# Kernel tuning notes

Measured on AMD Instinct MI355X. Metric: run time of the kernel, lower is better.

The kernel has to match this reference:

```python
import jax, jax.numpy as jnp
import numpy as np

MIN_SIGMA = 1e-3  # min_sigma from __init__
EPS = 1e-16


def rbf_kernel(A, B, sigma):
    """A: (bs, n, d), B: (m, d) -> K: (bs, n, m) with K = exp(-||a-b||^2 / (2 sigma^2))."""
    s = jnp.maximum(sigma, MIN_SIGMA)
    a2 = jnp.sum(A * A, axis=-1, keepdims=True)              # (bs, n, 1)
    b2 = jnp.sum(B * B, axis=-1)                             # (m,)
    d2 = a2 + b2[None, None, :] - 2.0 * jnp.einsum('bnd,md->bnm', A, B)
    d2 = jnp.maximum(d2, 0.0)
    return jnp.exp(-d2 / (2.0 * s * s))


def setup_inputs() -> dict:
    key = jax.random.key(0)
    k1, k2, k3 = jax.random.split(key, 3)
    BS, N, DX, DY, M = 256, 128, 32, 10, 2048  # batch, items(bag), dim_x, dim_y, n_comp
    inputs = jax.random.normal(k1, (BS, N, DX), dtype=jnp.float32)
    c_x = jax.random.normal(k2, (M, DX), dtype=jnp.float32)
    c_y = jax.random.uniform(k3, (M, DY), dtype=jnp.float32)
    comp_w = jnp.full((M,), 1.0 / M, dtype=jnp.float32)
    # sigma chosen ~ sqrt(dim_x) so RBF values don't underflow for Gaussian inputs
    sigma = jnp.float32(8.0)
    return {"inputs": inputs, "sigma": sigma, "c_x": c_x, "c_y": c_y, "comp_w": comp_w}


def reference(inputs, sigma, c_x, c_y, comp_w):
    bs, n, _ = inputs.shape
    # comp2dm: uniform bag weights w, components = inputs
    w = jnp.full((bs, n), 1.0 / n, dtype=inputs.dtype)       # (bs, n)
    # KQMUnit: kernel measurement
    K = rbf_kernel(inputs, c_x, sigma)                        # (bs, n, n_comp)
    out_w = jnp.einsum('bn,bnm->bm', w, comp_w[None, None, :] * (K * K))  # (bs, n_comp)
    out_w_sum = jnp.sum(out_w, axis=-1, keepdims=True)
    y_w = out_w / jnp.where(out_w_sum == 0, EPS, out_w_sum)   # normalized mixture weights
    # dm2comp + row-normalize components (batch-independent c_y)
    y_v = c_y / jnp.linalg.norm(c_y, axis=-1, keepdims=True)  # (n_comp, dim_y)
    # probs = einsum('...j,...ji->...i', y_w, y_v**2)
    probs = jnp.einsum('bm,md->bd', y_w, y_v * y_v)           # (bs, dim_y)
    return probs
```

## Files before the change

kernel.cpp:

```cpp
#include <hip/hip_runtime.h>
#include <hip/hip_bf16.h>

#define BS     256
#define N_BAG  128
#define DXD    32
#define DYD    10
#define M_COMP 2048
#define NTILES 8
#define WAVES  16
#define MT_PW  8

typedef __attribute__((ext_vector_type(8))) short short8v;
typedef __attribute__((ext_vector_type(4))) float f32x4;

static __device__ __forceinline__ unsigned int pkbf(float a, float b) {
    unsigned short ha = __bfloat16_as_ushort(__float2bfloat16(a));
    unsigned short hb = __bfloat16_as_ushort(__float2bfloat16(b));
    return (unsigned int)ha | ((unsigned int)hb << 16);
}
static __device__ __forceinline__ float fast_exp2(float x) {
#if __has_builtin(__builtin_amdgcn_exp2f)
    return __builtin_amdgcn_exp2f(x);
#else
    return __expf(x * 0.6931471805599453f);
#endif
}

__global__ __launch_bounds__(1024, 4) void fused_kernel(
    const float* __restrict__ X,
    const float* __restrict__ sig_p,
    const float* __restrict__ c_x,
    const float* __restrict__ c_y,
    const float* __restrict__ comp_w,
    float* __restrict__ out)
{
    __shared__ short8v XhiF[NTILES][64];
    __shared__ float   a2part[N_BAG][4];
    __shared__ float   a2buf[N_BAG];
    __shared__ float   red[WAVES][DYD + 2];
    __shared__ float   sm[DYD + 1];

    const int tid = threadIdx.x;
    const int b   = blockIdx.x;

    if (tid < 512) {
        const int n = tid >> 2, g4 = tid & 3;
        const float4* Xr = (const float4*)(X + ((size_t)(b * N_BAG + n) * DXD + 8 * g4));
        float4 v0 = Xr[0], v1 = Xr[1];
        float s = 0.f;
        s = fmaf(v0.x, v0.x, s); s = fmaf(v0.y, v0.y, s);
        s = fmaf(v0.z, v0.z, s); s = fmaf(v0.w, v0.w, s);
        s = fmaf(v1.x, v1.x, s); s = fmaf(v1.y, v1.y, s);
        s = fmaf(v1.z, v1.z, s); s = fmaf(v1.w, v1.w, s);
        union { unsigned int u[4]; short8v s8; } cv;
        cv.u[0] = pkbf(v0.x, v0.y); cv.u[1] = pkbf(v0.z, v0.w);
        cv.u[2] = pkbf(v1.x, v1.y); cv.u[3] = pkbf(v1.z, v1.w);
        XhiF[n >> 4][g4 * 16 + (n & 15)] = cv.s8;
        a2part[n][g4] = s;
    }
    __syncthreads();
    if (tid < N_BAG)
        a2buf[tid] = -0.5f * (a2part[tid][0] + a2part[tid][1] +
                              a2part[tid][2] + a2part[tid][3]);
    __syncthreads();

    const int lane = tid & 63, wv = tid >> 6;
    const int r = lane & 15, gq = lane >> 4;
    const int rowg = gq * 4;
    short8v Ah[NTILES];
    f32x4   a2f[NTILES];
#pragma unroll
    for (int t = 0; t < NTILES; ++t) {
        Ah[t]  = XhiF[t][lane];
        a2f[t] = *(const f32x4*)&a2buf[t * 16 + rowg];
    }

    const float sgm = fmaxf(sig_p[0], 1e-3f);
    const float cp  = 2.0f * 1.4426950408889634f / (sgm * sgm);

    float acc11[DYD + 1];
#pragma unroll
    for (int v = 0; v <= DYD; ++v) acc11[v] = 0.f;

    const int    m_base = wv * (MT_PW * 16) + r;
    const float* cxp    = c_x + (size_t)m_base * DXD + 8 * gq;

    float4 p0 = *(const float4*)(cxp);
    float4 p1 = *(const float4*)(cxp + 4);

#pragma unroll
    for (int i = 0; i < MT_PW; ++i) {
        const int m = m_base + 16 * i;
        float4 q0, q1;
        if (i + 1 < MT_PW) {
            q0 = *(const float4*)(cxp + (i + 1) * 16 * DXD);
            q1 = *(const float4*)(cxp + (i + 1) * 16 * DXD + 4);
        }
        const float cw = comp_w[m] * (1.0f / N_BAG);
        float cy[DYD];
        if (lane < 16) {
#pragma unroll
            for (int d = 0; d < DYD; ++d) cy[d] = c_y[(size_t)m * DYD + d];
        }
        union { unsigned int u[4]; short8v s8; } bc;
        bc.u[0] = pkbf(p0.x, p0.y); bc.u[1] = pkbf(p0.z, p0.w);
        bc.u[2] = pkbf(p1.x, p1.y); bc.u[3] = pkbf(p1.z, p1.w);
        float s = 0.f;
        s = fmaf(p0.x, p0.x, s); s = fmaf(p0.y, p0.y, s);
        s = fmaf(p0.z, p0.z, s); s = fmaf(p0.w, p0.w, s);
        s = fmaf(p1.x, p1.x, s); s = fmaf(p1.y, p1.y, s);
        s = fmaf(p1.z, p1.z, s); s = fmaf(p1.w, p1.w, s);
        s += __shfl_xor(s, 16, 64);
        s += __shfl_xor(s, 32, 64);
        const float cb = -0.5f * cp * s;

        float csum = 0.f;
#pragma unroll
        for (int t = 0; t < NTILES; ++t) {
            f32x4 acc = __builtin_amdgcn_mfma_f32_16x16x32_bf16(Ah[t], bc.s8, a2f[t], 0, 0, 0);
#pragma unroll
            for (int rr = 0; rr < 4; ++rr) {
                float e = fminf(fmaf(cp, acc[rr], cb), 0.f);
                csum += fast_exp2(e);
            }
        }
        csum += __shfl_xor(csum, 16, 64);
        csum += __shfl_xor(csum, 32, 64);

        if (lane < 16) {
            float ny = 0.f;
#pragma unroll
            for (int d = 0; d < DYD; ++d) ny = fmaf(cy[d], cy[d], ny);
            const float owm = csum * cw;
            const float yw  = owm * __builtin_amdgcn_rcpf(ny);
            acc11[0] += owm;
#pragma unroll
            for (int d = 0; d < DYD; ++d)
                acc11[1 + d] = fmaf(cy[d] * cy[d], yw, acc11[1 + d]);
        }
        p0 = q0; p1 = q1;
    }

#pragma unroll
    for (int v = 0; v <= DYD; ++v) {
        float x = acc11[v];
#pragma unroll
        for (int off = 32; off > 0; off >>= 1) x += __shfl_down(x, off, 64);
        if (lane == 0) red[wv][v] = x;
    }
    __syncthreads();
    if (tid <= DYD) {
        float ssum = 0.f;
#pragma unroll
        for (int w = 0; w < WAVES; ++w) ssum += red[w][tid];
        sm[tid] = ssum;
    }
    __syncthreads();
    if (tid < DYD) {
        float d = sm[0];
        d = (d == 0.f) ? 1e-16f : d;
        out[(size_t)b * DYD + tid] = sm[1 + tid] / d;
    }
}

extern "C" void kernel_launch(void* const* d_in, const int* in_sizes, int n_in,
                              void* d_out, int out_size, void* d_ws, size_t ws_size,
                              hipStream_t stream) {
    const float* X      = (const float*)d_in[0];
    const float* sigma  = (const float*)d_in[1];
    const float* c_x    = (const float*)d_in[2];
    const float* c_y    = (const float*)d_in[3];
    const float* comp_w = (const float*)d_in[4];
    float*       out    = (float*)d_out;

    fused_kernel<<<BS, 1024, 0, stream>>>(X, sigma, c_x, c_y, comp_w, out);
}
```

Before: 25.68 us.

## Split component dimension across blocks with two-kernel partial-sum reduction

Launches 8 blocks of 256 threads per batch row, each covering a 256-component chunk instead of one 1024-thread block per row, then combines per-chunk partial sums in a second small kernel. The scale and bias are folded into the bf16 A operand and the MFMA accumulator seed, which removes the per-element fma and clamp before exp2. The c_y reduction is moved to one component per thread with coalesced loads. This aims at better occupancy and load balance, at the cost of recomputing X prep per chunk, an extra launch, and dropping the clamp of the squared distance at zero.

```diff
diff --git a/kernel.cpp b/kernel.cpp
--- a/kernel.cpp
+++ b/kernel.cpp
@@ -6,9 +6,7 @@
 #define DXD    32
 #define DYD    10
 #define M_COMP 2048
-#define NTILES 8
-#define WAVES  16
-#define MT_PW  8
+#define CHUNKS 8
 
 typedef __attribute__((ext_vector_type(8))) short short8v;
 typedef __attribute__((ext_vector_type(4))) float f32x4;
@@ -26,25 +24,33 @@
 #endif
 }
 
-__global__ __launch_bounds__(1024, 4) void fused_kernel(
+__global__ __launch_bounds__(256, 8) void main_kernel(
     const float* __restrict__ X,
     const float* __restrict__ sig_p,
     const float* __restrict__ c_x,
     const float* __restrict__ c_y,
     const float* __restrict__ comp_w,
-    float* __restrict__ out)
+    float* __restrict__ part)
 {
-    __shared__ short8v XhiF[NTILES][64];
+    __shared__ short8v Af[8][64];
     __shared__ float   a2part[N_BAG][4];
-    __shared__ float   a2buf[N_BAG];
-    __shared__ float   red[WAVES][DYD + 2];
-    __shared__ float   sm[DYD + 1];
+    __shared__ float   a2c[N_BAG];
+    __shared__ float   ow_s[2][256];
+    __shared__ float   red[4][12];
 
-    const int tid = threadIdx.x;
-    const int b   = blockIdx.x;
+    const int tid   = threadIdx.x;
+    const int bid   = blockIdx.x;
+    const int b     = bid >> 3;
+    const int chunk = bid & 7;
 
-    if (tid < 512) {
-        const int n = tid >> 2, g4 = tid & 3;
+    const float sgm = fmaxf(sig_p[0], 1e-3f);
+    const float c2  = -1.4426950408889634f / (sgm * sgm);
+    const float sA  = -2.0f * c2;
+
+#pragma unroll
+    for (int k = 0; k < 2; ++k) {
+        const int u = tid + 256 * k;
+        const int n = u >> 2, g4 = u & 3;
         const float4* Xr = (const float4*)(X + ((size_t)(b * N_BAG + n) * DXD + 8 * g4));
         float4 v0 = Xr[0], v1 = Xr[1];
         float s = 0.f;
@@ -52,59 +58,39 @@
         s = fmaf(v0.z, v0.z, s); s = fmaf(v0.w, v0.w, s);
         s = fmaf(v1.x, v1.x, s); s = fmaf(v1.y, v1.y, s);
         s = fmaf(v1.z, v1.z, s); s = fmaf(v1.w, v1.w, s);
-        union { unsigned int u[4]; short8v s8; } cv;
-        cv.u[0] = pkbf(v0.x, v0.y); cv.u[1] = pkbf(v0.z, v0.w);
-        cv.u[2] = pkbf(v1.x, v1.y); cv.u[3] = pkbf(v1.z, v1.w);
-        XhiF[n >> 4][g4 * 16 + (n & 15)] = cv.s8;
+        union { unsigned int u4[4]; short8v s8; } cv;
+        cv.u4[0] = pkbf(sA * v0.x, sA * v0.y); cv.u4[1] = pkbf(sA * v0.z, sA * v0.w);
+        cv.u4[2] = pkbf(sA * v1.x, sA * v1.y); cv.u4[3] = pkbf(sA * v1.z, sA * v1.w);
+        Af[n >> 4][g4 * 16 + (n & 15)] = cv.s8;
         a2part[n][g4] = s;
     }
     __syncthreads();
     if (tid < N_BAG)
-        a2buf[tid] = -0.5f * (a2part[tid][0] + a2part[tid][1] +
-                              a2part[tid][2] + a2part[tid][3]);
+        a2c[tid] = c2 * (a2part[tid][0] + a2part[tid][1] +
+                         a2part[tid][2] + a2part[tid][3]);
     __syncthreads();
 
     const int lane = tid & 63, wv = tid >> 6;
-    const int r = lane & 15, gq = lane >> 4;
-    const int rowg = gq * 4;
-    short8v Ah[NTILES];
-    f32x4   a2f[NTILES];
+    const int half = wv & 1, wp = wv >> 1;
+    const int r = lane & 15, gq = lane >> 4, rowg = gq * 4;
+
+    short8v Xf[4];
+    f32x4   s4[4];
 #pragma unroll
-    for (int t = 0; t < NTILES; ++t) {
-        Ah[t]  = XhiF[t][lane];
-        a2f[t] = *(const f32x4*)&a2buf[t * 16 + rowg];
+    for (int j = 0; j < 4; ++j) {
+        Xf[j] = Af[half * 4 + j][lane];
+        s4[j] = *(const f32x4*)&a2c[(half * 4 + j) * 16 + rowg];
     }
 
-    const float sgm = fmaxf(sig_p[0], 1e-3f);
-    const float cp  = 2.0f * 1.4426950408889634f / (sgm * sgm);
-
-    float acc11[DYD + 1];
+    const int mt_base = chunk * 16 + wp * 8;
 #pragma unroll
-    for (int v = 0; v <= DYD; ++v) acc11[v] = 0.f;
-
-    const int    m_base = wv * (MT_PW * 16) + r;
-    const float* cxp    = c_x + (size_t)m_base * DXD + 8 * gq;
-
-    float4 p0 = *(const float4*)(cxp);
-    float4 p1 = *(const float4*)(cxp + 4);
-
-#pragma unroll
-    for (int i = 0; i < MT_PW; ++i) {
-        const int m = m_base + 16 * i;
-        float4 q0, q1;
-        if (i + 1 < MT_PW) {
-            q0 = *(const float4*)(cxp + (i + 1) * 16 * DXD);
-            q1 = *(const float4*)(cxp + (i + 1) * 16 * DXD + 4);
-        }
-        const float cw = comp_w[m] * (1.0f / N_BAG);
-        float cy[DYD];
-        if (lane < 16) {
-#pragma unroll
-            for (int d = 0; d < DYD; ++d) cy[d] = c_y[(size_t)m * DYD + d];
-        }
-        union { unsigned int u[4]; short8v s8; } bc;
-        bc.u[0] = pkbf(p0.x, p0.y); bc.u[1] = pkbf(p0.z, p0.w);
-        bc.u[2] = pkbf(p1.x, p1.y); bc.u[3] = pkbf(p1.z, p1.w);
+    for (int i = 0; i < 8; ++i) {
+        const int m = (mt_base + i) * 16 + r;
+        const float4* cp4 = (const float4*)(c_x + (size_t)m * DXD + 8 * gq);
+        float4 p0 = cp4[0], p1 = cp4[1];
+        union { unsigned int u4[4]; short8v s8; } bc;
+        bc.u4[0] = pkbf(p0.x, p0.y); bc.u4[1] = pkbf(p0.z, p0.w);
+        bc.u4[2] = pkbf(p1.x, p1.y); bc.u4[3] = pkbf(p1.z, p1.w);
         float s = 0.f;
         s = fmaf(p0.x, p0.x, s); s = fmaf(p0.y, p0.y, s);
         s = fmaf(p0.z, p0.z, s); s = fmaf(p0.w, p0.w, s);
@@ -112,54 +98,76 @@
         s = fmaf(p1.z, p1.z, s); s = fmaf(p1.w, p1.w, s);
         s += __shfl_xor(s, 16, 64);
         s += __shfl_xor(s, 32, 64);
-        const float cb = -0.5f * cp * s;
+        const float cbv = c2 * s;
 
-        float csum = 0.f;
+        float cs0 = 0.f, cs1 = 0.f;
 #pragma unroll
-        for (int t = 0; t < NTILES; ++t) {
-            f32x4 acc = __builtin_amdgcn_mfma_f32_16x16x32_bf16(Ah[t], bc.s8, a2f[t], 0, 0, 0);
-#pragma unroll
-            for (int rr = 0; rr < 4; ++rr) {
-                float e = fminf(fmaf(cp, acc[rr], cb), 0.f);
-                csum += fast_exp2(e);
-            }
+        for (int j = 0; j < 4; ++j) {
+            f32x4 seed = s4[j] + cbv;
+            f32x4 acc  = __builtin_amdgcn_mfma_f32_16x16x32_bf16(Xf[j], bc.s8, seed, 0, 0, 0);
+            cs0 += fast_exp2(acc[0]); cs1 += fast_exp2(acc[1]);
+            cs0 += fast_exp2(acc[2]); cs1 += fast_exp2(acc[3]);
         }
+        float csum = cs0 + cs1;
         csum += __shfl_xor(csum, 16, 64);
         csum += __shfl_xor(csum, 32, 64);
+        if (lane < 16) ow_s[half][wp * 128 + i * 16 + r] = csum;
+    }
+    __syncthreads();
 
-        if (lane < 16) {
-            float ny = 0.f;
+    {
+        const int m = chunk * 256 + tid;
+        const float w = (ow_s[0][tid] + ow_s[1][tid]) * comp_w[m] * (1.0f / N_BAG);
+        const float2* cyp = (const float2*)(c_y + (size_t)m * DYD);
+        float2 y0 = cyp[0], y1 = cyp[1], y2 = cyp[2], y3 = cyp[3], y4 = cyp[4];
+        float cy[DYD] = {y0.x, y0.y, y1.x, y1.y, y2.x, y2.y, y3.x, y3.y, y4.x, y4.y};
+        float ny = 0.f;
 #pragma unroll
-            for (int d = 0; d < DYD; ++d) ny = fmaf(cy[d], cy[d], ny);
-            const float owm = csum * cw;
-            const float yw  = owm * __builtin_amdgcn_rcpf(ny);
-            acc11[0] += owm;
+        for (int d = 0; d < DYD; ++d) ny = fmaf(cy[d], cy[d], ny);
+        const float yw = w * __builtin_amdgcn_rcpf(ny);
+        float vals[DYD + 1];
+        vals[0] = w;
 #pragma unroll
-            for (int d = 0; d < DYD; ++d)
-                acc11[1 + d] = fmaf(cy[d] * cy[d], yw, acc11[1 + d]);
-        }
-        p0 = q0; p1 = q1;
-    }
+        for (int d = 0; d < DYD; ++d) vals[1 + d] = yw * cy[d] * cy[d];
 
 #pragma unroll
+        for (int v = 0; v <= DYD; ++v) {
+            float x = vals[v];
+#pragma unroll
+            for (int off = 32; off > 0; off >>= 1) x += __shfl_down(x, off, 64);
+            if (lane == 0) red[wv][v] = x;
+        }
+        __syncthreads();
+        if (tid <= DYD)
+            part[(size_t)bid * 16 + tid] = red[0][tid] + red[1][tid] + red[2][tid] + red[3][tid];
+    }
+}
+
+__global__ __launch_bounds__(1024) void combine_kernel(const float* __restrict__ part,
+                                                       float* __restrict__ out) {
+    const int t = threadIdx.x;
+    const int b = t >> 2, q = t & 3;
+    float s[DYD + 1];
+#pragma unroll
+    for (int v = 0; v <= DYD; ++v) s[v] = 0.f;
+#pragma unroll
+    for (int c = 0; c < 2; ++c) {
+        const float* p = part + (size_t)(b * 8 + q + 4 * c) * 16;
+#pragma unroll
+        for (int v = 0; v <= DYD; ++v) s[v] += p[v];
+    }
+#pragma unroll
     for (int v = 0; v <= DYD; ++v) {
-        float x = acc11[v];
+        s[v] += __shfl_xor(s[v], 1, 64);
+        s[v] += __shfl_xor(s[v], 2, 64);
+    }
+    if (q == 0) {
+        float d = s[0];
+        d = (d == 0.f) ? 1e-16f : d;
+        const float inv = 1.0f / d;
 #pragma unroll
-        for (int off = 32; off > 0; off >>= 1) x += __shfl_down(x, off, 64);
-        if (lane == 0) red[wv][v] = x;
-    }
-    __syncthreads();
-    if (tid <= DYD) {
-        float ssum = 0.f;
-#pragma unroll
-        for (int w = 0; w < WAVES; ++w) ssum += red[w][tid];
-        sm[tid] = ssum;
-    }
-    __syncthreads();
-    if (tid < DYD) {
-        float d = sm[0];
-        d = (d == 0.f) ? 1e-16f : d;
-        out[(size_t)b * DYD + tid] = sm[1 + tid] / d;
+        for (int dd = 0; dd < DYD; ++dd)
+            out[(size_t)b * DYD + dd] = s[1 + dd] * inv;
     }
 }
 
@@ -173,5 +181,8 @@
     const float* comp_w = (const float*)d_in[4];
     float*       out    = (float*)d_out;
 
-    fused_kernel<<<BS, 1024, 0, stream>>>(X, sigma, c_x, c_y, comp_w, out);
+    float* part = (float*)d_ws;
+
+    main_kernel<<<BS * CHUNKS, 256, 0, stream>>>(X, sigma, c_x, c_y, comp_w, part);
+    combine_kernel<<<1, 1024, 0, stream>>>(part, out);
 }
```

After: 31.33 us. +22.0%, slower.

## Factor column norm out of exponent and split epilogue into parallel LDS pass

Applied to the files above, without the earlier changes.

Scales X by the exponent constant before the bf16 pack and folds the row norm into the MFMA accumulator init, so the MFMA output feeds exp2 directly without the per-element fma and clamp. The per-component term exp(-|c|^2/(2s^2)) times the component weight is computed once per block into LDS. The per-wave c_y epilogue, which kept 48 of 64 lanes idle, is replaced by an extra barrier and a pass over all 2048 components spread across 1024 threads. In exchange every block recomputes all 2048 c_x norms, dropping the clamp risks small precision differences, and LDS use grows by 16KB.

```diff
diff --git a/kernel.cpp b/kernel.cpp
--- a/kernel.cpp
+++ b/kernel.cpp
@@ -34,14 +34,20 @@
     const float* __restrict__ comp_w,
     float* __restrict__ out)
 {
-    __shared__ short8v XhiF[NTILES][64];
+    __shared__ short8v Af[NTILES][64];
     __shared__ float   a2part[N_BAG][4];
-    __shared__ float   a2buf[N_BAG];
-    __shared__ float   red[WAVES][DYD + 2];
-    __shared__ float   sm[DYD + 1];
+    __shared__ float   a2c[N_BAG];
+    __shared__ float   ebw[M_COMP];
+    __shared__ float   ow_s[M_COMP];
+    __shared__ float   red[WAVES][12];
+    __shared__ float   sm[12];
 
     const int tid = threadIdx.x;
     const int b   = blockIdx.x;
+
+    const float sgm = fmaxf(sig_p[0], 1e-3f);
+    const float c2  = -1.4426950408889634f / (sgm * sgm);
+    const float sA  = -2.0f * c2;
 
     if (tid < 512) {
         const int n = tid >> 2, g4 = tid & 3;
@@ -52,35 +58,40 @@
         s = fmaf(v0.z, v0.z, s); s = fmaf(v0.w, v0.w, s);
         s = fmaf(v1.x, v1.x, s); s = fmaf(v1.y, v1.y, s);
         s = fmaf(v1.z, v1.z, s); s = fmaf(v1.w, v1.w, s);
-        union { unsigned int u[4]; short8v s8; } cv;
-        cv.u[0] = pkbf(v0.x, v0.y); cv.u[1] = pkbf(v0.z, v0.w);
-        cv.u[2] = pkbf(v1.x, v1.y); cv.u[3] = pkbf(v1.z, v1.w);
-        XhiF[n >> 4][g4 * 16 + (n & 15)] = cv.s8;
+        union { unsigned int u4[4]; short8v s8; } cv;
+        cv.u4[0] = pkbf(sA * v0.x, sA * v0.y); cv.u4[1] = pkbf(sA * v0.z, sA * v0.w);
+        cv.u4[2] = pkbf(sA * v1.x, sA * v1.y); cv.u4[3] = pkbf(sA * v1.z, sA * v1.w);
+        Af[n >> 4][g4 * 16 + (n & 15)] = cv.s8;
         a2part[n][g4] = s;
+    }
+#pragma unroll
+    for (int k = 0; k < 2; ++k) {
+        const int m = tid + 1024 * k;
+        const float4* cp = (const float4*)(c_x + (size_t)m * DXD);
+        float s = 0.f;
+#pragma unroll
+        for (int j = 0; j < 8; ++j) {
+            float4 v = cp[j];
+            s = fmaf(v.x, v.x, s); s = fmaf(v.y, v.y, s);
+            s = fmaf(v.z, v.z, s); s = fmaf(v.w, v.w, s);
+        }
+        ebw[m] = fast_exp2(c2 * s) * comp_w[m] * (1.0f / N_BAG);
     }
     __syncthreads();
     if (tid < N_BAG)
-        a2buf[tid] = -0.5f * (a2part[tid][0] + a2part[tid][1] +
-                              a2part[tid][2] + a2part[tid][3]);
+        a2c[tid] = c2 * (a2part[tid][0] + a2part[tid][1] +
+                         a2part[tid][2] + a2part[tid][3]);
     __syncthreads();
 
     const int lane = tid & 63, wv = tid >> 6;
-    const int r = lane & 15, gq = lane >> 4;
-    const int rowg = gq * 4;
+    const int r = lane & 15, gq = lane >> 4, rowg = gq * 4;
     short8v Ah[NTILES];
     f32x4   a2f[NTILES];
 #pragma unroll
     for (int t = 0; t < NTILES; ++t) {
-        Ah[t]  = XhiF[t][lane];
-        a2f[t] = *(const f32x4*)&a2buf[t * 16 + rowg];
+        Ah[t]  = Af[t][lane];
+        a2f[t] = *(const f32x4*)&a2c[t * 16 + rowg];
     }
-
-    const float sgm = fmaxf(sig_p[0], 1e-3f);
-    const float cp  = 2.0f * 1.4426950408889634f / (sgm * sgm);
-
-    float acc11[DYD + 1];
-#pragma unroll
-    for (int v = 0; v <= DYD; ++v) acc11[v] = 0.f;
 
     const int    m_base = wv * (MT_PW * 16) + r;
     const float* cxp    = c_x + (size_t)m_base * DXD + 8 * gq;
@@ -90,70 +101,61 @@
 
 #pragma unroll
     for (int i = 0; i < MT_PW; ++i) {
-        const int m = m_base + 16 * i;
         float4 q0, q1;
         if (i + 1 < MT_PW) {
             q0 = *(const float4*)(cxp + (i + 1) * 16 * DXD);
             q1 = *(const float4*)(cxp + (i + 1) * 16 * DXD + 4);
         }
-        const float cw = comp_w[m] * (1.0f / N_BAG);
-        float cy[DYD];
-        if (lane < 16) {
-#pragma unroll
-            for (int d = 0; d < DYD; ++d) cy[d] = c_y[(size_t)m * DYD + d];
-        }
-        union { unsigned int u[4]; short8v s8; } bc;
-        bc.u[0] = pkbf(p0.x, p0.y); bc.u[1] = pkbf(p0.z, p0.w);
-        bc.u[2] = pkbf(p1.x, p1.y); bc.u[3] = pkbf(p1.z, p1.w);
-        float s = 0.f;
-        s = fmaf(p0.x, p0.x, s); s = fmaf(p0.y, p0.y, s);
-        s = fmaf(p0.z, p0.z, s); s = fmaf(p0.w, p0.w, s);
-        s = fmaf(p1.x, p1.x, s); s = fmaf(p1.y, p1.y, s);
-        s = fmaf(p1.z, p1.z, s); s = fmaf(p1.w, p1.w, s);
-        s += __shfl_xor(s, 16, 64);
-        s += __shfl_xor(s, 32, 64);
-        const float cb = -0.5f * cp * s;
+        union { unsigned int u4[4]; short8v s8; } bc;
+        bc.u4[0] = pkbf(p0.x, p0.y); bc.u4[1] = pkbf(p0.z, p0.w);
+        bc.u4[2] = pkbf(p1.x, p1.y); bc.u4[3] = pkbf(p1.z, p1.w);
 
-        float csum = 0.f;
+        float cs0 = 0.f, cs1 = 0.f, cs2 = 0.f, cs3 = 0.f;
 #pragma unroll
         for (int t = 0; t < NTILES; ++t) {
             f32x4 acc = __builtin_amdgcn_mfma_f32_16x16x32_bf16(Ah[t], bc.s8, a2f[t], 0, 0, 0);
-#pragma unroll
-            for (int rr = 0; rr < 4; ++rr) {
-                float e = fminf(fmaf(cp, acc[rr], cb), 0.f);
-                csum += fast_exp2(e);
-            }
+            cs0 += fast_exp2(acc[0]); cs1 += fast_exp2(acc[1]);
+            cs2 += fast_exp2(acc[2]); cs3 += fast_exp2(acc[3]);
         }
+        float csum = (cs0 + cs1) + (cs2 + cs3);
         csum += __shfl_xor(csum, 16, 64);
         csum += __shfl_xor(csum, 32, 64);
-
-        if (lane < 16) {
-            float ny = 0.f;
-#pragma unroll
-            for (int d = 0; d < DYD; ++d) ny = fmaf(cy[d], cy[d], ny);
-            const float owm = csum * cw;
-            const float yw  = owm * __builtin_amdgcn_rcpf(ny);
-            acc11[0] += owm;
-#pragma unroll
-            for (int d = 0; d < DYD; ++d)
-                acc11[1 + d] = fmaf(cy[d] * cy[d], yw, acc11[1 + d]);
-        }
+        if (lane < 16) ow_s[m_base + 16 * i] = csum;
         p0 = q0; p1 = q1;
     }
+    __syncthreads();
 
+    float vals[DYD + 1];
+#pragma unroll
+    for (int v = 0; v <= DYD; ++v) vals[v] = 0.f;
+#pragma unroll
+    for (int k = 0; k < 2; ++k) {
+        const int m = tid + 1024 * k;
+        const float w = ow_s[m] * ebw[m];
+        const float2* cyp = (const float2*)(c_y + (size_t)m * DYD);
+        float2 y0 = cyp[0], y1 = cyp[1], y2 = cyp[2], y3 = cyp[3], y4 = cyp[4];
+        float cy[DYD] = {y0.x, y0.y, y1.x, y1.y, y2.x, y2.y, y3.x, y3.y, y4.x, y4.y};
+        float ny = 0.f;
+#pragma unroll
+        for (int d = 0; d < DYD; ++d) ny = fmaf(cy[d], cy[d], ny);
+        const float yw = w * __builtin_amdgcn_rcpf(ny);
+        vals[0] += w;
+#pragma unroll
+        for (int d = 0; d < DYD; ++d) vals[1 + d] = fmaf(yw, cy[d] * cy[d], vals[1 + d]);
+    }
 #pragma unroll
     for (int v = 0; v <= DYD; ++v) {
-        float x = acc11[v];
+        float x = vals[v];
 #pragma unroll
         for (int off = 32; off > 0; off >>= 1) x += __shfl_down(x, off, 64);
         if (lane == 0) red[wv][v] = x;
     }
     __syncthreads();
     if (tid <= DYD) {
-        float ssum = 0.f;
+        float s = 0.f;
 #pragma unroll
-        for (int w = 0; w < WAVES; ++w) ssum += red[w][tid];
-        sm[tid] = ssum;
+        for (int w16 = 0; w16 < WAVES; ++w16) s += red[w16][tid];
+        sm[tid] = s;
     }
     __syncthreads();
     if (tid < DYD) {
```

Result: slower. 26.49 us (+3.1%).
